# Performance work log

Measured on AMD Instinct MI355X. Metric: run time of the kernel, lower is better.

The kernel has to match this reference:

```python
import jax, jax.numpy as jnp
import numpy as np

N = 4096
M = 1024
APPERTURE = 250
L1, L2, L3, PRED = 1024, 512, 128, 1
EPS = 1e-6


def _layer_norm(x, gamma, beta):
    # torch x.std(-1) is unbiased (ddof=1)
    mean = jnp.mean(x, axis=-1, keepdims=True)
    std = jnp.std(x, axis=-1, ddof=1, keepdims=True)
    return gamma * (x - mean) / (std + EPS) + beta


def _self_attention(x, Wq, Wk, Wv, Wo, band_mask):
    # x: [n, m]; Linear(bias=False) => x @ W.T
    K = x @ Wk.T
    Q = (x @ Wq.T) * 0.06
    V = x @ Wv.T
    logits = Q @ K.T                      # [n, n]
    logits = jnp.where(band_mask, logits, -jnp.inf)  # keep |i-j| < apperture
    att = jax.nn.softmax(logits, axis=-1)
    # original: y = (V^T @ att)^T == att^T @ V  (note the transpose!)
    y = att.T @ V
    return y @ Wo.T, att


def setup_inputs() -> dict:
    key = jax.random.key(0)
    ks = jax.random.split(key, 20)
    s = 0.02
    inp = {
        'x1': jax.random.normal(ks[0], (1, N, M), jnp.float32),
        'x2': jax.random.normal(ks[1], (1, N, M), jnp.float32),
        'x3': jax.random.normal(ks[2], (1, N, M), jnp.float32),
        'Wq': jax.random.normal(ks[3], (M, M), jnp.float32) * s,
        'Wk': jax.random.normal(ks[4], (M, M), jnp.float32) * s,
        'Wv': jax.random.normal(ks[5], (M, M), jnp.float32) * s,
        'Wo': jax.random.normal(ks[6], (M, M), jnp.float32) * s,
        'ka_w': jax.random.normal(ks[7], (L1, M), jnp.float32) * s,
        'ka_b': jnp.zeros((L1,), jnp.float32),
        'kb_w': jax.random.normal(ks[8], (L2, L1), jnp.float32) * s,
        'kb_b': jnp.zeros((L2,), jnp.float32),
        'kc_w': jax.random.normal(ks[9], (L3, L2), jnp.float32) * s,
        'kc_b': jnp.zeros((L3,), jnp.float32),
        'kd_w': jax.random.normal(ks[10], (PRED, L3), jnp.float32) * s,
        'kd_b': jnp.zeros((PRED,), jnp.float32),
        'g13': jnp.ones((M,), jnp.float32),
        'b13': jnp.zeros((M,), jnp.float32),
        'gkc': jnp.ones((L3,), jnp.float32),
        'bkc': jnp.zeros((L3,), jnp.float32),
        'seq_len': N,
    }
    return inp


def reference(x1, x2, x3, Wq, Wk, Wv, Wo, ka_w, ka_b, kb_w, kb_b, kc_w, kc_b,
              kd_w, kd_b, g13, b13, gkc, bkc, seq_len):
    x1 = x1.reshape(-1, x1.shape[2])
    x2 = x2.reshape(-1, x2.shape[2])
    x3 = x3.reshape(-1, x3.shape[2])
    n = x1.shape[0]
    idx = jnp.arange(n)
    band_mask = jnp.abs(idx[:, None] - idx[None, :]) < APPERTURE  # allowed

    y1, att1 = _self_attention(x1, Wq, Wk, Wv, Wo, band_mask)
    y2, _ = _self_attention(x2, Wq, Wk, Wv, Wo, band_mask)
    y3, _ = _self_attention(x3, Wq, Wk, Wv, Wo, band_mask)

    # residual + (dropout == identity in eval) + shared LayerNorm
    y1 = _layer_norm(y1 + x1, g13, b13)
    y2 = _layer_norm(y2 + x2, g13, b13)
    y3 = _layer_norm(y3 + x3, g13, b13)

    y = y1 + y2 + y3  # cmb == [1,1,1]
    y = y @ ka_w.T + ka_b
    y = y @ kb_w.T + kb_b
    y = jax.nn.relu(y @ kc_w.T + kc_b)
    y = _layer_norm(y, gkc, bkc)
    y = jax.nn.sigmoid(y @ kd_w.T + kd_b)
    return y.reshape(1, -1), att1
```

## Files before the change

### kernel.cpp

```cpp
#include <hip/hip_runtime.h>
#include <hip/hip_bf16.h>
#include <cstdint>
#include <cstddef>

#define NSEQ 4096
#define MDIM 1024

typedef __attribute__((ext_vector_type(8))) short short8;
typedef __attribute__((ext_vector_type(4))) float f32x4;
typedef __attribute__((ext_vector_type(2))) long long2v;
typedef __attribute__((ext_vector_type(8))) int int8v;
typedef __attribute__((ext_vector_type(4))) int int4v;

typedef const __attribute__((address_space(1))) void gvoid_t;
typedef __attribute__((address_space(3))) void lvoid_t;

__device__ __forceinline__ unsigned short f2b(float x) {
  union { float f; unsigned int u; } a; a.f = x;
  unsigned int r = (a.u + 0x7fffu + ((a.u >> 16) & 1u)) >> 16;
  return (unsigned short)r;
}
__device__ __forceinline__ float b2f(unsigned short u) {
  union { float f; unsigned int u32; } a; a.u32 = ((unsigned int)u) << 16;
  return a.f;
}
__device__ __forceinline__ unsigned char f2e4(float x) {
  return (unsigned char)(__builtin_amdgcn_cvt_pk_fp8_f32(x, x, 0, false) & 0xff);
}
__device__ __forceinline__ unsigned int f2e4x4(float a, float b, float c, float d) {
  unsigned int lo = __builtin_amdgcn_cvt_pk_fp8_f32(a, b, 0, false);
  return (unsigned int)__builtin_amdgcn_cvt_pk_fp8_f32(c, d, lo, true);
}

__device__ __forceinline__ int8v pack32(const unsigned char* p0,
                                        const unsigned char* p1) {
  int4v lo = *(const int4v*)p0;
  int4v hi = *(const int4v*)p1;
  int8v r;
  r[0] = lo[0]; r[1] = lo[1]; r[2] = lo[2]; r[3] = lo[3];
  r[4] = hi[0]; r[5] = hi[1]; r[6] = hi[2]; r[7] = hi[3];
  return r;
}

__global__ __launch_bounds__(256) void k_cvt_all(
    const float* __restrict__ s0, const float* __restrict__ s1,
    const float* __restrict__ s2, const float* __restrict__ s3,
    const float* __restrict__ s4, const float* __restrict__ s5,
    const float* __restrict__ s6,
    const float* __restrict__ xa, const float* __restrict__ xb,
    const float* __restrict__ xc,
    unsigned char* __restrict__ Wf8, unsigned short* __restrict__ Wmlp,
    unsigned char* __restrict__ Xdst, float* __restrict__ sums) {
  int idx = blockIdx.x * 256 + threadIdx.x;
  if (idx < 1048576) {
    int seg = idx >> 18, local = idx & 262143;
    const float* src = (seg == 0) ? s0 : (seg == 1) ? s1 : (seg == 2) ? s2 : s3;
    float4 v = *(const float4*)(src + (size_t)local * 4);
    *(unsigned int*)(Wf8 + (size_t)idx * 4) =
        f2e4x4(v.x * 64.f, v.y * 64.f, v.z * 64.f, v.w * 64.f);
  } else if (idx < 1458176) {
    int i2 = idx - 1048576;
    const float* src; int local;
    if (i2 < 262144) { src = s4; local = i2; }
    else if (i2 < 393216) { src = s5; local = i2 - 262144; }
    else { src = s6; local = i2 - 393216; }
    float4 v = *(const float4*)(src + (size_t)local * 4);
    ushort4 o; o.x = f2b(v.x); o.y = f2b(v.y); o.z = f2b(v.z); o.w = f2b(v.w);
    *(ushort4*)(Wmlp + (size_t)i2 * 4) = o;
  } else if (idx < 4603904) {
    int i2 = idx - 1458176;
    int seg = i2 >> 20, local = i2 & 1048575;
    const float* src = (seg == 0) ? xa : (seg == 1) ? xb : xc;
    float4 v = *(const float4*)(src + (size_t)local * 4);
    *(unsigned int*)(Xdst + (size_t)i2 * 4) = f2e4x4(v.x, v.y, v.z, v.w);
  } else {
    int i3 = idx - 4603904;
    *(float4*)(sums + (size_t)i3 * 4) = make_float4(0.f, 0.f, 0.f, 0.f);
  }
}

__global__ __launch_bounds__(256) void k_gemm(
    const unsigned char* __restrict__ A, int lda,
    const unsigned char* __restrict__ B, int ldb,
    void* __restrict__ Cout, void* __restrict__ Cout2, int ldc,
    int K, float alpha, int okind, int do_exp, int mode,
    const unsigned char* __restrict__ A1, const unsigned char* __restrict__ A2,
    float* __restrict__ sums_out) {
  __shared__ unsigned char smem[2 * 128 * 128];
  unsigned char* As = smem;
  unsigned char* Bs = smem + 128 * 128;
  int bx = blockIdx.x, by = blockIdx.y;
  const unsigned char* Ab;
  const unsigned char* Bb;
  void* Cdst = Cout;
  int k0 = 0, k1 = K, b_koff = 0;
  int ldce = ldc;
  int rbase, cbase;
  int ldae = lda, ldbe = ldb;
  if (mode == 0) {
    Ab = A + (size_t)by * 128 * lda;
    Bb = B + (size_t)bx * 128 * ldb;
    rbase = bx * 128; cbase = by * 128;
  } else if (mode == 3) {
    if (by < 16) {
      Ab = A + (size_t)by * 128 * lda;
      Bb = B + (size_t)bx * 128 * ldb;
      if (by >= 8) Cdst = Cout2;
      rbase = bx * 128; cbase = (by & 7) * 128;
    } else {
      Ab = B + (size_t)bx * 128 * ldb;
      Bb = A1 + (size_t)(by - 16) * 128 * 1024;
      Cdst = (void*)const_cast<unsigned char*>(A2);
      rbase = (by - 16) * 128; cbase = bx * 128;
      ldce = 3 * NSEQ;
    }
  } else if (mode == 1) {
    int s = bx >> 5, ti = bx & 31;
    int bt = ti + by - 2;
    if (bt < 0 || bt >= 32) return;
    Ab = A + (size_t)(s * 32 + bt) * 128 * lda;
    Bb = B + (size_t)bx * 128 * ldb;
    rbase = bx * 128; cbase = by * 128;
  } else {
    int s = bx >> 5, ti = bx & 31;
    Ab = A + (size_t)by * 128 * lda + s * NSEQ;
    const unsigned char* Bbase = (s == 0) ? B : ((s == 1) ? A1 : A2);
    Bb = Bbase + (size_t)ti * 128 * 640;
    ldbe = 640;
    int lo = ti - 2; if (lo < 0) lo = 0;
    int hi = ti + 3; if (hi > 32) hi = 32;
    k0 = lo * 128; k1 = hi * 128;
    b_koff = (ti - 2) * 128;
    rbase = bx * 128; cbase = by * 128;
  }

  const int t = threadIdx.x;
  const int l = t & 63;
  const int w = t >> 6;
  const int fr = l & 15;
  const int quad = l >> 4;
  const int wm = (w >> 1) * 64;
  const int wn = (w & 1) * 64;
  const int fq4 = quad * 4;

  int srow[4], scg[4], sloff[4];
#pragma unroll
  for (int j = 0; j < 4; j++) {
    srow[j] = w * 32 + j * 8 + (l >> 3);
    scg[j] = ((l & 7) - srow[j]) & 7;
    sloff[j] = (w * 32 + j * 8) * 128 + l * 16;
  }

  f32x4 acc[4][4];
#pragma unroll
  for (int m = 0; m < 4; m++)
#pragma unroll
    for (int n = 0; n < 4; n++) acc[m][n] = (f32x4){0.f, 0.f, 0.f, 0.f};

  const int c0 = quad * 2;
  for (int kk = k0; kk < k1; kk += 128) {
    int kb = kk - b_koff;
    __syncthreads();
#pragma unroll
    for (int j = 0; j < 4; j++)
      __builtin_amdgcn_global_load_lds(
          (gvoid_t*)(Ab + (size_t)srow[j] * ldae + kk + scg[j] * 16),
          (lvoid_t*)(As + sloff[j]), 16, 0, 0);
#pragma unroll
    for (int j = 0; j < 4; j++)
      __builtin_amdgcn_global_load_lds(
          (gvoid_t*)(Bb + (size_t)srow[j] * ldbe + kb + scg[j] * 16),
          (lvoid_t*)(Bs + sloff[j]), 16, 0, 0);
    __syncthreads();
    {
      int8v a8[4], b8[4];
#pragma unroll
      for (int m = 0; m < 4; m++) {
        int r = wm + m * 16 + fr;
        int s0i = (c0 + r) & 7, s1i = (s0i + 1) & 7;
        a8[m] = pack32(As + r * 128 + s0i * 16, As + r * 128 + s1i * 16);
      }
#pragma unroll
      for (int n = 0; n < 4; n++) {
        int r = wn + n * 16 + fr;
        int s0i = (c0 + r) & 7, s1i = (s0i + 1) & 7;
        b8[n] = pack32(Bs + r * 128 + s0i * 16, Bs + r * 128 + s1i * 16);
      }
#pragma unroll
      for (int m = 0; m < 4; m++)
#pragma unroll
        for (int n = 0; n < 4; n++)
          acc[m][n] = __builtin_amdgcn_mfma_scale_f32_16x16x128_f8f6f4(
              a8[m], b8[n], acc[m][n], 0, 0, 0, 0x7F7F7F7F, 0, 0x7F7F7F7F);
    }
  }

  float rowsum[4] = {0.f, 0.f, 0.f, 0.f};
  const int jb = (mode == 1) ? ((bx & 31) - 2) * 128 : 0;
#pragma unroll
  for (int m = 0; m < 4; m++) {
#pragma unroll
    for (int n = 0; n < 4; n++) {
      int oc = cbase + wm + m * 16 + fq4;
      int orow = rbase + wn + n * 16 + fr;
      float v0 = acc[m][n][0] * alpha, v1 = acc[m][n][1] * alpha;
      float v2 = acc[m][n][2] * alpha, v3 = acc[m][n][3] * alpha;
      if (okind == 1) {
        if (do_exp) {
          v0 = __expf(v0); v1 = __expf(v1); v2 = __expf(v2); v3 = __expf(v3);
          if (mode == 1) {
            int d0 = (orow & 4095) - (jb + oc);
            rowsum[n] += ((unsigned)(d0 + 249) < 499u ? v0 : 0.f)
                       + ((unsigned)(d0 + 248) < 499u ? v1 : 0.f)
                       + ((unsigned)(d0 + 247) < 499u ? v2 : 0.f)
                       + ((unsigned)(d0 + 246) < 499u ? v3 : 0.f);
          }
        }
        ushort4 o; o.x = f2b(v0); o.y = f2b(v1); o.z = f2b(v2); o.w = f2b(v3);
        *(uint2*)((unsigned short*)Cdst + (size_t)orow * ldce + oc) = *(uint2*)&o;
      } else if (okind == 2) {
        *(unsigned int*)((unsigned char*)Cdst + (size_t)orow * ldce + oc) =
            f2e4x4(v0, v1, v2, v3);
      } else {
        *(float4*)((float*)Cdst + (size_t)orow * ldce + oc) = make_float4(v0, v1, v2, v3);
      }
    }
  }
  if (mode == 1 && do_exp) {
#pragma unroll
    for (int n = 0; n < 4; n++) {
      float sv = rowsum[n];
      sv += __shfl_xor(sv, 16);
      sv += __shfl_xor(sv, 32);
      if (quad == 0) {
        int orow = rbase + wn + n * 16 + fr;
        atomicAdd(sums_out + orow, sv);
      }
    }
  }
}

__global__ __launch_bounds__(256) void k_gemm64(
    const unsigned short* __restrict__ A, int lda,
    const unsigned short* __restrict__ B, int ldb,
    void* __restrict__ Cout, int ldc, int K,
    const float* __restrict__ bias, int relu, int out_bf16) {
  __shared__ unsigned short smem[4 * 64 * 64];
  int bx = blockIdx.x, by = blockIdx.y;
  const unsigned short* Ab = A + (size_t)by * 64 * lda;
  const unsigned short* Bb = B + (size_t)bx * 64 * ldb;
  int rbase = bx * 64, cbase = by * 64;

  const int t = threadIdx.x;
  const int l = t & 63;
  const int w = t >> 6;
  const int fr = l & 15;
  const int quad = l >> 4;
  const int wm = (w & 1) * 32;
  const int wn = (w >> 1) * 32;
  const int fq4 = quad * 4;

  int srow[2], scg[2], sloff[2];
#pragma unroll
  for (int j = 0; j < 2; j++) {
    srow[j] = w * 16 + j * 8 + (l >> 3);
    scg[j] = ((l & 7) - srow[j]) & 7;
    sloff[j] = (w * 16 + j * 8) * 64 + l * 8;
  }

  f32x4 acc[2][2];
#pragma unroll
  for (int m = 0; m < 2; m++)
#pragma unroll
    for (int n = 0; n < 2; n++) acc[m][n] = (f32x4){0.f, 0.f, 0.f, 0.f};

  const int nt = K >> 6;

#pragma unroll
  for (int j = 0; j < 2; j++)
    __builtin_amdgcn_global_load_lds(
        (gvoid_t*)(Ab + (size_t)srow[j] * lda + scg[j] * 8),
        (lvoid_t*)(smem + sloff[j]), 16, 0, 0);
#pragma unroll
  for (int j = 0; j < 2; j++)
    __builtin_amdgcn_global_load_lds(
        (gvoid_t*)(Bb + (size_t)srow[j] * ldb + scg[j] * 8),
        (lvoid_t*)(smem + 4096 + sloff[j]), 16, 0, 0);

  for (int tt = 0; tt < nt; tt++) {
    __syncthreads();
    if (tt + 1 < nt) {
      int kk = (tt + 1) * 64;
      unsigned short* Asn = smem + ((tt + 1) & 1) * 8192;
#pragma unroll
      for (int j = 0; j < 2; j++)
        __builtin_amdgcn_global_load_lds(
            (gvoid_t*)(Ab + (size_t)srow[j] * lda + kk + scg[j] * 8),
            (lvoid_t*)(Asn + sloff[j]), 16, 0, 0);
#pragma unroll
      for (int j = 0; j < 2; j++)
        __builtin_amdgcn_global_load_lds(
            (gvoid_t*)(Bb + (size_t)srow[j] * ldb + kk + scg[j] * 8),
            (lvoid_t*)(Asn + 4096 + sloff[j]), 16, 0, 0);
    }
    const unsigned short* Asc = smem + (tt & 1) * 8192;
    const unsigned short* Bsc = Asc + 4096;
#pragma unroll
    for (int s = 0; s < 2; s++) {
      short8 af[2], bf[2];
#pragma unroll
      for (int m = 0; m < 2; m++) {
        int r = wm + m * 16 + fr;
        int slot = (s * 4 + quad + r) & 7;
        af[m] = *(const short8*)(Asc + r * 64 + slot * 8);
      }
#pragma unroll
      for (int n = 0; n < 2; n++) {
        int r = wn + n * 16 + fr;
        int slot = (s * 4 + quad + r) & 7;
        bf[n] = *(const short8*)(Bsc + r * 64 + slot * 8);
      }
#pragma unroll
      for (int m = 0; m < 2; m++)
#pragma unroll
        for (int n = 0; n < 2; n++)
          acc[m][n] = __builtin_amdgcn_mfma_f32_16x16x32_bf16(af[m], bf[n], acc[m][n], 0, 0, 0);
    }
  }

#pragma unroll
  for (int m = 0; m < 2; m++) {
#pragma unroll
    for (int n = 0; n < 2; n++) {
      int oc = cbase + wm + m * 16 + fq4;
      int orow = rbase + wn + n * 16 + fr;
      float4 bv = bias ? *(const float4*)(bias + oc) : make_float4(0.f, 0.f, 0.f, 0.f);
      float v0 = acc[m][n][0] + bv.x, v1 = acc[m][n][1] + bv.y;
      float v2 = acc[m][n][2] + bv.z, v3 = acc[m][n][3] + bv.w;
      if (relu) {
        v0 = fmaxf(v0, 0.f); v1 = fmaxf(v1, 0.f);
        v2 = fmaxf(v2, 0.f); v3 = fmaxf(v3, 0.f);
      }
      if (out_bf16) {
        ushort4 o; o.x = f2b(v0); o.y = f2b(v1); o.z = f2b(v2); o.w = f2b(v3);
        *(uint2*)((unsigned short*)Cout + (size_t)orow * ldc + oc) = *(uint2*)&o;
      } else {
        *(float4*)((float*)Cout + (size_t)orow * ldc + oc) = make_float4(v0, v1, v2, v3);
      }
    }
  }
}

__global__ __launch_bounds__(256) void k_build_attT(const unsigned short* __restrict__ Eband,
                                                    const float* __restrict__ sums,
                                                    unsigned char* __restrict__ t0,
                                                    unsigned char* __restrict__ t1,
                                                    unsigned char* __restrict__ t2) {
  int byy = blockIdx.y;
  int s = byy >> 5, ti = byy & 31;
  int tj = ti + (int)blockIdx.x - 2;
  if (tj < 0 || tj >= 32) return;
  unsigned char* dst = (s == 0) ? t0 : ((s == 1) ? t1 : t2);
  __shared__ unsigned char T[128][132];
  int t = threadIdx.x;
  int c0 = (ti - tj + 2) * 128;
  int colg = (t & 31) * 4;
  for (int jj = t >> 5; jj < 128; jj += 8) {
    int jg = s * NSEQ + tj * 128 + jj;
    float inv = 16.f / sums[jg];
    ushort4 v = *(const ushort4*)&Eband[(size_t)jg * 640 + c0 + colg];
    float vv[4] = {b2f(v.x), b2f(v.y), b2f(v.z), b2f(v.w)};
#pragma unroll
    for (int q = 0; q < 4; q++) {
      int i = ti * 128 + colg + q;
      int d = i - (tj * 128 + jj);
      float a = (d < 250 && d > -250) ? vv[q] * inv : 0.f;
      T[colg + q][jj] = f2e4(a);
    }
  }
  __syncthreads();
  int jb0 = (tj - ti + 2) * 128;
  for (int ii = t >> 5; ii < 128; ii += 8) {
    size_t o = (size_t)(ti * 128 + ii) * 640 + jb0 + colg;
    *(unsigned int*)(dst + o) = *(const unsigned int*)&T[ii][colg];
  }
}

__global__ __launch_bounds__(256) void k_write_att(const unsigned short* __restrict__ Eband,
                                                   const float* __restrict__ sums,
                                                   float* __restrict__ att) {
  int i = blockIdx.x;
  int ti = i >> 7, cbase = (ti - 2) * 128;
  int jlo = i - 249; if (jlo < 0) jlo = 0;
  int jhi = i + 249; if (jhi > NSEQ - 1) jhi = NSEQ - 1;
  float inv = 1.f / sums[i];
  const unsigned short* L = Eband + (size_t)i * 640;
  float* arow = att + (size_t)i * NSEQ;
  for (int j0 = threadIdx.x * 4; j0 < NSEQ; j0 += 1024) {
    float ov[4];
#pragma unroll
    for (int q = 0; q < 4; q++) {
      int j = j0 + q;
      ov[q] = (j >= jlo && j <= jhi) ? b2f(L[j - cbase]) * inv : 0.f;
    }
    *(float4*)(arow + j0) = make_float4(ov[0], ov[1], ov[2], ov[3]);
  }
}

__global__ __launch_bounds__(256) void k_ln3(const unsigned short* __restrict__ yo,
                                             const float* __restrict__ x1,
                                             const float* __restrict__ x2,
                                             const float* __restrict__ x3,
                                             const float* __restrict__ g,
                                             const float* __restrict__ b,
                                             unsigned short* __restrict__ ysum_b) {
  int i = blockIdx.x, t = threadIdx.x;
  int w = t >> 6, lane = t & 63;
  __shared__ float red[8];
  const float* xs[3] = {x1, x2, x3};
  float4 gg = *(const float4*)(g + t * 4);
  float4 bb = *(const float4*)(b + t * 4);
  float acc[4] = {0.f, 0.f, 0.f, 0.f};
  for (int s = 0; s < 3; s++) {
    ushort4 yv = *(const ushort4*)(yo + ((size_t)(s * NSEQ + i)) * MDIM + t * 4);
    float4 xx = *(const float4*)(xs[s] + (size_t)i * MDIM + t * 4);
    float v[4] = {b2f(yv.x) + xx.x, b2f(yv.y) + xx.y, b2f(yv.z) + xx.z, b2f(yv.w) + xx.w};
    float s1 = v[0] + v[1] + v[2] + v[3];
    float s2 = v[0]*v[0] + v[1]*v[1] + v[2]*v[2] + v[3]*v[3];
    for (int off = 32; off; off >>= 1) { s1 += __shfl_xor(s1, off); s2 += __shfl_xor(s2, off); }
    __syncthreads();
    if (lane == 0) { red[w] = s1; red[4 + w] = s2; }
    __syncthreads();
    float S1 = red[0] + red[1] + red[2] + red[3];
    float S2 = red[4] + red[5] + red[6] + red[7];
    float mean = S1 * (1.f / 1024.f);
    float var = (S2 - S1 * mean) * (1.f / 1023.f);
    float rstd = 1.f / (sqrtf(var) + 1e-6f);
    acc[0] += gg.x * (v[0] - mean) * rstd + bb.x;
    acc[1] += gg.y * (v[1] - mean) * rstd + bb.y;
    acc[2] += gg.z * (v[2] - mean) * rstd + bb.z;
    acc[3] += gg.w * (v[3] - mean) * rstd + bb.w;
  }
  ushort4 o;
  o.x = f2b(acc[0]); o.y = f2b(acc[1]); o.z = f2b(acc[2]); o.w = f2b(acc[3]);
  *(ushort4*)(ysum_b + (size_t)i * MDIM + t * 4) = o;
}

__global__ __launch_bounds__(128) void k_final(const float* __restrict__ h3,
                                               const float* __restrict__ g,
                                               const float* __restrict__ b,
                                               const float* __restrict__ kdw,
                                               const float* __restrict__ kdb,
                                               float* __restrict__ yout) {
  int i = blockIdx.x, t = threadIdx.x;
  float v = h3[(size_t)i * 128 + t];
  float s1 = v, s2 = v * v;
  for (int off = 32; off; off >>= 1) { s1 += __shfl_xor(s1, off); s2 += __shfl_xor(s2, off); }
  __shared__ float red[4];
  int w = t >> 6, lane = t & 63;
  if (lane == 0) { red[w] = s1; red[2 + w] = s2; }
  __syncthreads();
  float S1 = red[0] + red[1], S2 = red[2] + red[3];
  float mean = S1 * (1.f / 128.f);
  float var = (S2 - S1 * mean) * (1.f / 127.f);
  float rstd = 1.f / (sqrtf(var) + 1e-6f);
  float ln = g[t] * (v - mean) * rstd + b[t];
  float p = ln * kdw[t];
  for (int off = 32; off; off >>= 1) p += __shfl_xor(p, off);
  __syncthreads();
  if (lane == 0) red[w] = p;
  __syncthreads();
  if (t == 0) {
    float z = red[0] + red[1] + kdb[0];
    yout[i] = 1.f / (1.f + __expf(-z));
  }
}

extern "C" void kernel_launch(void* const* d_in, const int* in_sizes, int n_in,
                              void* d_out, int out_size, void* d_ws, size_t ws_size,
                              hipStream_t stream) {
  const float* x1 = (const float*)d_in[0];
  const float* x2 = (const float*)d_in[1];
  const float* x3 = (const float*)d_in[2];
  const float* Wq = (const float*)d_in[3];
  const float* Wk = (const float*)d_in[4];
  const float* Wv = (const float*)d_in[5];
  const float* Wo = (const float*)d_in[6];
  const float* ka_w = (const float*)d_in[7];
  const float* ka_b = (const float*)d_in[8];
  const float* kb_w = (const float*)d_in[9];
  const float* kb_b = (const float*)d_in[10];
  const float* kc_w = (const float*)d_in[11];
  const float* kc_b = (const float*)d_in[12];
  const float* kd_w = (const float*)d_in[13];
  const float* kd_b = (const float*)d_in[14];
  const float* g13 = (const float*)d_in[15];
  const float* b13 = (const float*)d_in[16];
  const float* gkc = (const float*)d_in[17];
  const float* bkc = (const float*)d_in[18];

  float* y_out = (float*)d_out;
  float* att_out = y_out + NSEQ;

  char* ws = (char*)d_ws;
  size_t off = 0;
  auto alloc = [&](size_t bytes) -> void* {
    void* p = ws + off;
    off += (bytes + 255) & ~(size_t)255;
    return p;
  };
  const size_t NM = (size_t)3 * NSEQ * MDIM;
  unsigned char* Wf = (unsigned char*)alloc(4 * 1048576);
  unsigned short* Wmlp = (unsigned short*)alloc((1048576 + 524288 + 65536) * 2);
  unsigned char* Xf = (unsigned char*)alloc(NM);
  unsigned char* Qf = (unsigned char*)alloc(NM);
  unsigned char* Kf = (unsigned char*)alloc(NM);
  unsigned char* VTf = (unsigned char*)alloc(NM);
  unsigned short* Eband = (unsigned short*)alloc((size_t)3 * NSEQ * 640 * 2);
  float* sums = (float*)alloc((size_t)3 * NSEQ * 4);
  unsigned char* aT0 = (unsigned char*)alloc((size_t)NSEQ * 640);
  unsigned char* aT1 = (unsigned char*)alloc((size_t)NSEQ * 640);
  unsigned char* aT2 = (unsigned char*)alloc((size_t)NSEQ * 640);
  unsigned char* Wv_f = Wf + 2097152;
  unsigned char* Wo_f = Wf + 3145728;
  unsigned short* ka_b16 = Wmlp;
  unsigned short* kb_b16 = Wmlp + 1048576;
  unsigned short* kc_b16 = Wmlp + 1572864;
  unsigned char* yb = Xf;
  unsigned short* yo = (unsigned short*)Qf;
  unsigned short* ysum_b = (unsigned short*)VTf;
  unsigned short* h1b = (unsigned short*)Xf;
  unsigned short* h2b = (unsigned short*)Qf;
  float* h3 = (float*)aT0;

  k_cvt_all<<<17996, 256, 0, stream>>>(Wq, Wk, Wv, Wo, ka_w, kb_w, kc_w,
                                       x1, x2, x3, Wf, Wmlp, Xf, sums);

  k_gemm<<<dim3(96, 24), 256, 0, stream>>>(Wf, 1024, Xf, 1024, Qf, Kf, 1024,
                                           1024, 1.f / 64.f, 2, 0, 3, Wv_f, VTf, nullptr);
  k_gemm<<<dim3(96, 5), 256, 0, stream>>>(Kf, 1024, Qf, 1024, Eband, nullptr, 640,
                                          1024, 0.06f, 1, 1, 1, nullptr, nullptr, sums);
  k_build_attT<<<dim3(5, 96), 256, 0, stream>>>(Eband, sums, aT0, aT1, aT2);
  k_gemm<<<dim3(96, 8), 256, 0, stream>>>(VTf, 3 * NSEQ, aT0, 640, yb, nullptr, 1024,
                                          NSEQ, 0.5f, 2, 0, 2, aT1, aT2, nullptr);
  k_write_att<<<4096, 256, 0, stream>>>(Eband, sums, att_out);
  k_gemm<<<dim3(96, 8), 256, 0, stream>>>(Wo_f, 1024, yb, 1024, yo, nullptr, 1024,
                                          1024, 1.f / 512.f, 1, 0, 0, nullptr, nullptr, nullptr);
  k_ln3<<<4096, 256, 0, stream>>>(yo, x1, x2, x3, g13, b13, ysum_b);

  k_gemm64<<<dim3(64, 16), 256, 0, stream>>>(ka_b16, 1024, ysum_b, 1024, h1b, 1024,
                                             1024, ka_b, 0, 1);
  k_gemm64<<<dim3(64, 8), 256, 0, stream>>>(kb_b16, 1024, h1b, 1024, h2b, 512,
                                            1024, kb_b, 0, 1);
  k_gemm64<<<dim3(64, 2), 256, 0, stream>>>(kc_b16, 512, h2b, 512, h3, 128,
                                            512, kc_b, 1, 0);
  k_final<<<4096, 128, 0, stream>>>(h3, gkc, bkc, kd_w, kd_b, y_out);
}
```

Measured before the change: 344.0 us.

## Template FP8 GEMM per call site and double-buffer LDS tiles

Turns the generic runtime-dispatched FP8 GEMM kernel into a template specialised on mode, output kind and exp flag, with one thin kernel per call site, which removes runtime branches and dead epilogue code. For the logits, AV and output-projection GEMMs it adds double-buffered LDS staging (64 KB shared), issuing the next tile's global-to-LDS loads before computing on the current tile so memory latency overlaps MFMA work. The larger shared-memory footprint may reduce occupancy. The QKV GEMM stays single-buffered.

```diff
diff --git a/kernel.cpp b/kernel.cpp
--- a/kernel.cpp
+++ b/kernel.cpp
@@ -79,16 +79,14 @@
   }
 }
 
-__global__ __launch_bounds__(256) void k_gemm(
+template <int MODE, int OKIND, int DO_EXP, int DBUF>
+__device__ __forceinline__ void gemm_core(
     const unsigned char* __restrict__ A, int lda,
     const unsigned char* __restrict__ B, int ldb,
     void* __restrict__ Cout, void* __restrict__ Cout2, int ldc,
-    int K, float alpha, int okind, int do_exp, int mode,
+    int K, float alpha,
     const unsigned char* __restrict__ A1, const unsigned char* __restrict__ A2,
-    float* __restrict__ sums_out) {
-  __shared__ unsigned char smem[2 * 128 * 128];
-  unsigned char* As = smem;
-  unsigned char* Bs = smem + 128 * 128;
+    float* __restrict__ sums_out, unsigned char* __restrict__ smem) {
   int bx = blockIdx.x, by = blockIdx.y;
   const unsigned char* Ab;
   const unsigned char* Bb;
@@ -97,11 +95,11 @@
   int ldce = ldc;
   int rbase, cbase;
   int ldae = lda, ldbe = ldb;
-  if (mode == 0) {
+  if constexpr (MODE == 0) {
     Ab = A + (size_t)by * 128 * lda;
     Bb = B + (size_t)bx * 128 * ldb;
     rbase = bx * 128; cbase = by * 128;
-  } else if (mode == 3) {
+  } else if constexpr (MODE == 3) {
     if (by < 16) {
       Ab = A + (size_t)by * 128 * lda;
       Bb = B + (size_t)bx * 128 * ldb;
@@ -114,10 +112,9 @@
       rbase = (by - 16) * 128; cbase = bx * 128;
       ldce = 3 * NSEQ;
     }
-  } else if (mode == 1) {
+  } else if constexpr (MODE == 1) {
     int s = bx >> 5, ti = bx & 31;
     int bt = ti + by - 2;
-    if (bt < 0 || bt >= 32) return;
     Ab = A + (size_t)(s * 32 + bt) * 128 * lda;
     Bb = B + (size_t)bx * 128 * ldb;
     rbase = bx * 128; cbase = by * 128;
@@ -158,21 +155,77 @@
     for (int n = 0; n < 4; n++) acc[m][n] = (f32x4){0.f, 0.f, 0.f, 0.f};
 
   const int c0 = quad * 2;
-  for (int kk = k0; kk < k1; kk += 128) {
-    int kb = kk - b_koff;
-    __syncthreads();
-#pragma unroll
-    for (int j = 0; j < 4; j++)
-      __builtin_amdgcn_global_load_lds(
-          (gvoid_t*)(Ab + (size_t)srow[j] * ldae + kk + scg[j] * 16),
-          (lvoid_t*)(As + sloff[j]), 16, 0, 0);
-#pragma unroll
-    for (int j = 0; j < 4; j++)
-      __builtin_amdgcn_global_load_lds(
-          (gvoid_t*)(Bb + (size_t)srow[j] * ldbe + kb + scg[j] * 16),
-          (lvoid_t*)(Bs + sloff[j]), 16, 0, 0);
-    __syncthreads();
+
+  if constexpr (DBUF) {
+    const int nt = (k1 - k0) >> 7;
     {
+      int kk = k0, kb = kk - b_koff;
+#pragma unroll
+      for (int j = 0; j < 4; j++)
+        __builtin_amdgcn_global_load_lds(
+            (gvoid_t*)(Ab + (size_t)srow[j] * ldae + kk + scg[j] * 16),
+            (lvoid_t*)(smem + sloff[j]), 16, 0, 0);
+#pragma unroll
+      for (int j = 0; j < 4; j++)
+        __builtin_amdgcn_global_load_lds(
+            (gvoid_t*)(Bb + (size_t)srow[j] * ldbe + kb + scg[j] * 16),
+            (lvoid_t*)(smem + 16384 + sloff[j]), 16, 0, 0);
+    }
+    for (int tt = 0; tt < nt; tt++) {
+      __syncthreads();
+      if (tt + 1 < nt) {
+        int kk = k0 + (tt + 1) * 128, kb = kk - b_koff;
+        unsigned char* Asn = smem + ((tt + 1) & 1) * 32768;
+#pragma unroll
+        for (int j = 0; j < 4; j++)
+          __builtin_amdgcn_global_load_lds(
+              (gvoid_t*)(Ab + (size_t)srow[j] * ldae + kk + scg[j] * 16),
+              (lvoid_t*)(Asn + sloff[j]), 16, 0, 0);
+#pragma unroll
+        for (int j = 0; j < 4; j++)
+          __builtin_amdgcn_global_load_lds(
+              (gvoid_t*)(Bb + (size_t)srow[j] * ldbe + kb + scg[j] * 16),
+              (lvoid_t*)(Asn + 16384 + sloff[j]), 16, 0, 0);
+      }
+      const unsigned char* Asc = smem + (tt & 1) * 32768;
+      const unsigned char* Bsc = Asc + 16384;
+      int8v a8[4], b8[4];
+#pragma unroll
+      for (int m = 0; m < 4; m++) {
+        int r = wm + m * 16 + fr;
+        int s0i = (c0 + r) & 7, s1i = (s0i + 1) & 7;
+        a8[m] = pack32(Asc + r * 128 + s0i * 16, Asc + r * 128 + s1i * 16);
+      }
+#pragma unroll
+      for (int n = 0; n < 4; n++) {
+        int r = wn + n * 16 + fr;
+        int s0i = (c0 + r) & 7, s1i = (s0i + 1) & 7;
+        b8[n] = pack32(Bsc + r * 128 + s0i * 16, Bsc + r * 128 + s1i * 16);
+      }
+#pragma unroll
+      for (int m = 0; m < 4; m++)
+#pragma unroll
+        for (int n = 0; n < 4; n++)
+          acc[m][n] = __builtin_amdgcn_mfma_scale_f32_16x16x128_f8f6f4(
+              a8[m], b8[n], acc[m][n], 0, 0, 0, 0x7F7F7F7F, 0, 0x7F7F7F7F);
+    }
+  } else {
+    unsigned char* As = smem;
+    unsigned char* Bs = smem + 16384;
+    for (int kk = k0; kk < k1; kk += 128) {
+      int kb = kk - b_koff;
+      __syncthreads();
+#pragma unroll
+      for (int j = 0; j < 4; j++)
+        __builtin_amdgcn_global_load_lds(
+            (gvoid_t*)(Ab + (size_t)srow[j] * ldae + kk + scg[j] * 16),
+            (lvoid_t*)(As + sloff[j]), 16, 0, 0);
+#pragma unroll
+      for (int j = 0; j < 4; j++)
+        __builtin_amdgcn_global_load_lds(
+            (gvoid_t*)(Bb + (size_t)srow[j] * ldbe + kb + scg[j] * 16),
+            (lvoid_t*)(Bs + sloff[j]), 16, 0, 0);
+      __syncthreads();
       int8v a8[4], b8[4];
 #pragma unroll
       for (int m = 0; m < 4; m++) {
@@ -196,7 +249,7 @@
   }
 
   float rowsum[4] = {0.f, 0.f, 0.f, 0.f};
-  const int jb = (mode == 1) ? ((bx & 31) - 2) * 128 : 0;
+  const int jb = ((bx & 31) - 2) * 128;
 #pragma unroll
   for (int m = 0; m < 4; m++) {
 #pragma unroll
@@ -205,10 +258,10 @@
       int orow = rbase + wn + n * 16 + fr;
       float v0 = acc[m][n][0] * alpha, v1 = acc[m][n][1] * alpha;
       float v2 = acc[m][n][2] * alpha, v3 = acc[m][n][3] * alpha;
-      if (okind == 1) {
-        if (do_exp) {
+      if constexpr (OKIND == 1) {
+        if constexpr (DO_EXP) {
           v0 = __expf(v0); v1 = __expf(v1); v2 = __expf(v2); v3 = __expf(v3);
-          if (mode == 1) {
+          if constexpr (MODE == 1) {
             int d0 = (orow & 4095) - (jb + oc);
             rowsum[n] += ((unsigned)(d0 + 249) < 499u ? v0 : 0.f)
                        + ((unsigned)(d0 + 248) < 499u ? v1 : 0.f)
@@ -218,15 +271,13 @@
         }
         ushort4 o; o.x = f2b(v0); o.y = f2b(v1); o.z = f2b(v2); o.w = f2b(v3);
         *(uint2*)((unsigned short*)Cdst + (size_t)orow * ldce + oc) = *(uint2*)&o;
-      } else if (okind == 2) {
+      } else {
         *(unsigned int*)((unsigned char*)Cdst + (size_t)orow * ldce + oc) =
             f2e4x4(v0, v1, v2, v3);
-      } else {
-        *(float4*)((float*)Cdst + (size_t)orow * ldce + oc) = make_float4(v0, v1, v2, v3);
-      }
-    }
-  }
-  if (mode == 1 && do_exp) {
+      }
+    }
+  }
+  if constexpr (MODE == 1 && DO_EXP) {
 #pragma unroll
     for (int n = 0; n < 4; n++) {
       float sv = rowsum[n];
@@ -238,6 +289,43 @@
       }
     }
   }
+}
+
+__global__ __launch_bounds__(256) void k_qkv(
+    const unsigned char* __restrict__ A, const unsigned char* __restrict__ B,
+    void* __restrict__ Cout, void* __restrict__ Cout2, float alpha,
+    const unsigned char* __restrict__ A1, const unsigned char* __restrict__ A2) {
+  __shared__ unsigned char smem[2 * 128 * 128];
+  gemm_core<3, 2, 0, 0>(A, 1024, B, 1024, Cout, Cout2, 1024, 1024, alpha,
+                        A1, A2, nullptr, smem);
+}
+
+__global__ __launch_bounds__(256) void k_logits(
+    const unsigned char* __restrict__ A, const unsigned char* __restrict__ B,
+    void* __restrict__ Cout, float alpha, float* __restrict__ sums) {
+  int ti = blockIdx.x & 31;
+  int bt = ti + (int)blockIdx.y - 2;
+  if (bt < 0 || bt >= 32) return;
+  __shared__ unsigned char smem[4 * 128 * 128];
+  gemm_core<1, 1, 1, 1>(A, 1024, B, 1024, Cout, nullptr, 640, 1024, alpha,
+                        nullptr, nullptr, sums, smem);
+}
+
+__global__ __launch_bounds__(256) void k_av(
+    const unsigned char* __restrict__ A, const unsigned char* __restrict__ B,
+    void* __restrict__ Cout, float alpha,
+    const unsigned char* __restrict__ A1, const unsigned char* __restrict__ A2) {
+  __shared__ unsigned char smem[4 * 128 * 128];
+  gemm_core<2, 2, 0, 1>(A, 3 * NSEQ, B, 640, Cout, nullptr, 1024, NSEQ, alpha,
+                        A1, A2, nullptr, smem);
+}
+
+__global__ __launch_bounds__(256) void k_wo(
+    const unsigned char* __restrict__ A, const unsigned char* __restrict__ B,
+    void* __restrict__ Cout, float alpha) {
+  __shared__ unsigned char smem[4 * 128 * 128];
+  gemm_core<0, 1, 0, 1>(A, 1024, B, 1024, Cout, nullptr, 1024, 1024, alpha,
+                        nullptr, nullptr, nullptr, smem);
 }
 
 __global__ __launch_bounds__(256) void k_gemm64(
@@ -536,16 +624,12 @@
   k_cvt_all<<<17996, 256, 0, stream>>>(Wq, Wk, Wv, Wo, ka_w, kb_w, kc_w,
                                        x1, x2, x3, Wf, Wmlp, Xf, sums);
 
-  k_gemm<<<dim3(96, 24), 256, 0, stream>>>(Wf, 1024, Xf, 1024, Qf, Kf, 1024,
-                                           1024, 1.f / 64.f, 2, 0, 3, Wv_f, VTf, nullptr);
-  k_gemm<<<dim3(96, 5), 256, 0, stream>>>(Kf, 1024, Qf, 1024, Eband, nullptr, 640,
-                                          1024, 0.06f, 1, 1, 1, nullptr, nullptr, sums);
+  k_qkv<<<dim3(96, 24), 256, 0, stream>>>(Wf, Xf, Qf, Kf, 1.f / 64.f, Wv_f, VTf);
+  k_logits<<<dim3(96, 5), 256, 0, stream>>>(Kf, Qf, Eband, 0.06f, sums);
   k_build_attT<<<dim3(5, 96), 256, 0, stream>>>(Eband, sums, aT0, aT1, aT2);
-  k_gemm<<<dim3(96, 8), 256, 0, stream>>>(VTf, 3 * NSEQ, aT0, 640, yb, nullptr, 1024,
-                                          NSEQ, 0.5f, 2, 0, 2, aT1, aT2, nullptr);
+  k_av<<<dim3(96, 8), 256, 0, stream>>>(VTf, aT0, yb, 0.5f, aT1, aT2);
   k_write_att<<<4096, 256, 0, stream>>>(Eband, sums, att_out);
-  k_gemm<<<dim3(96, 8), 256, 0, stream>>>(Wo_f, 1024, yb, 1024, yo, nullptr, 1024,
-                                          1024, 1.f / 512.f, 1, 0, 0, nullptr, nullptr, nullptr);
+  k_wo<<<dim3(96, 8), 256, 0, stream>>>(Wo_f, yb, yo, 1.f / 512.f);
   k_ln3<<<4096, 256, 0, stream>>>(yo, x1, x2, x3, g13, b13, ysum_b);
 
   k_gemm64<<<dim3(64, 16), 256, 0, stream>>>(ka_b16, 1024, ysum_b, 1024, h1b, 1024,
```

Result: faster. 335.2 us (-2.5%).
